# Kernel tuning notes

Hardware: AMD Instinct MI355X
Metric: run time of the kernel (lower is better)

Reference implementation:

```python
import jax, jax.numpy as jnp
import numpy as np

ALPHA_MIN = 1e-6
TAU_EPS = 1e-3


def _spectral_normalize(W):
    # spectral_norm divides by the largest singular value of W
    sigma = jnp.linalg.svd(W, compute_uv=False)[0]
    return W / sigma


def setup_inputs() -> dict:
    key = jax.random.key(0)
    ks = jax.random.split(key, 10)
    B, T, D, k = 8, 8192, 128, 64
    x = jax.random.normal(ks[0], (B, T, D), dtype=jnp.float32)
    dt = jax.random.uniform(ks[1], (B, T), dtype=jnp.float32) * (2.0 / T)
    alpha_mod = 0.1 * jax.random.normal(ks[2], (B, T, k), dtype=jnp.float32)
    omega_mod = 0.1 * jax.random.normal(ks[3], (B, T, k), dtype=jnp.float32)
    tau_mod = 0.1 * jax.random.normal(ks[4], (B, T, 1), dtype=jnp.float32)
    s_real_raw = jax.random.normal(ks[5], (k,), dtype=jnp.float32)
    s_imag = jax.random.uniform(ks[6], (k,), dtype=jnp.float32, minval=-np.pi, maxval=np.pi)
    tau_raw = jnp.zeros((), dtype=jnp.float32)
    W = jax.random.normal(ks[7], (k, D), dtype=jnp.float32) * (1.0 / np.sqrt(D))
    b = jax.random.uniform(ks[8], (k,), dtype=jnp.float32, minval=-1.0 / np.sqrt(D), maxval=1.0 / np.sqrt(D))
    return {"x": x, "dt": dt, "alpha_mod": alpha_mod, "omega_mod": omega_mod,
            "tau_mod": tau_mod, "s_real_raw": s_real_raw, "s_imag": s_imag,
            "tau_raw": tau_raw, "W": W, "b": b}


def reference(x, dt, alpha_mod, omega_mod, tau_mod, s_real_raw, s_imag, tau_raw, W, b):
    # recurrent mode of LearnableLaplacianBasis
    B, T, D = x.shape
    k = s_imag.shape[0]
    W_sn = _spectral_normalize(W)
    u = jnp.einsum('btd,kd->btk', x, W_sn) + b  # [B,T,k]

    tau = jax.nn.softplus(tau_raw) + TAU_EPS
    alpha0 = (jax.nn.softplus(s_real_raw) + ALPHA_MIN) * tau  # [k]
    omega0 = s_imag * tau                                      # [k]

    alpha = alpha0 * jnp.exp(alpha_mod)   # [B,T,k]
    omega = omega0 * jnp.exp(omega_mod)
    scale = jnp.exp(tau_mod)              # [B,T,1] broadcasts to [B,T,k]
    alpha = alpha * scale
    omega = omega * scale

    dt_bt1 = dt[:, :, None]
    rho = jnp.exp(-alpha * dt_bt1)
    theta = omega * dt_bt1
    cos_t = jnp.cos(theta)
    sin_t = jnp.sin(theta)

    # time-major for scan: [T,B,k]
    xs = (jnp.swapaxes(rho, 0, 1), jnp.swapaxes(cos_t, 0, 1),
          jnp.swapaxes(sin_t, 0, 1), jnp.swapaxes(u, 0, 1))

    def step(carry, inp):
        c, s = carry
        r, ct, st, ut = inp
        c2 = r * (c * ct - s * st) + ut
        s2 = r * (c * st + s * ct)
        return (c2, s2), (c2, s2)

    init = (jnp.zeros((B, k), x.dtype), jnp.zeros((B, k), x.dtype))
    _, (C, S) = jax.lax.scan(step, init, xs)  # [T,B,k] each
    C = jnp.swapaxes(C, 0, 1)
    S = jnp.swapaxes(S, 0, 1)
    return jnp.concatenate([C, S], axis=2)  # [B,T,2k]
```

## Files before the change

### kernel.cpp

```cpp
#include <hip/hip_runtime.h>
#include <hip/hip_bf16.h>

#define B_   8
#define T_   8192
#define D_   128
#define K_   64
#define TC   16

#define GEMM_BLOCKS 1024
#define GP 136

typedef float  floatx4  __attribute__((ext_vector_type(4)));
typedef __bf16 bf16x8   __attribute__((ext_vector_type(8)));
typedef unsigned short ushortx8 __attribute__((ext_vector_type(8)));

__device__ inline unsigned short f2bf(float f) {
  unsigned u = __float_as_uint(f);
  u = u + 0x7FFFu + ((u >> 16) & 1u);
  return (unsigned short)(u >> 16);
}
__device__ inline float bf2f(unsigned short h) {
  return __uint_as_float(((unsigned)h) << 16);
}

#define MP 72

__global__ __launch_bounds__(256) void k_gemm_sigma(
    const float* __restrict__ x, const float* __restrict__ W,
    float* __restrict__ V, float* __restrict__ sig, int* __restrict__ FL) {
  __shared__ __align__(16) unsigned char smem[2 * 64 * GP * 2 + 512];

  const int tid  = threadIdx.x;
  const int lane = tid & 63;
  const int wv   = tid >> 6;
  const int l15  = lane & 15;
  const int q    = lane >> 4;

  if (blockIdx.x == GEMM_BLOCKS) {
    FL[tid] = 0;

    unsigned short* Ma = (unsigned short*)smem;
    unsigned short* Mb = Ma + 64 * MP;
    float* red = (float*)(smem + 2 * 64 * MP * 2);
    float* vsh = red + 4;
    int*   jsh = (int*)(vsh + 64);

    floatx4 acc[4] = {};
    const int arow = 16 * wv + l15;
    for (int s = 0; s < 4; ++s) {
      const int kb = 32 * s + 8 * q;
      float4 a0 = *(const float4*)(W + arow * 128 + kb);
      float4 a1 = *(const float4*)(W + arow * 128 + kb + 4);
      ushortx8 ua;
      ua[0] = f2bf(a0.x); ua[1] = f2bf(a0.y); ua[2] = f2bf(a0.z); ua[3] = f2bf(a0.w);
      ua[4] = f2bf(a1.x); ua[5] = f2bf(a1.y); ua[6] = f2bf(a1.z); ua[7] = f2bf(a1.w);
      bf16x8 av = __builtin_bit_cast(bf16x8, ua);
      for (int tn = 0; tn < 4; ++tn) {
        const int brow = 16 * tn + l15;
        float4 b0 = *(const float4*)(W + brow * 128 + kb);
        float4 b1 = *(const float4*)(W + brow * 128 + kb + 4);
        ushortx8 ub;
        ub[0] = f2bf(b0.x); ub[1] = f2bf(b0.y); ub[2] = f2bf(b0.z); ub[3] = f2bf(b0.w);
        ub[4] = f2bf(b1.x); ub[5] = f2bf(b1.y); ub[6] = f2bf(b1.z); ub[7] = f2bf(b1.w);
        bf16x8 bv = __builtin_bit_cast(bf16x8, ub);
        acc[tn] = __builtin_amdgcn_mfma_f32_16x16x32_bf16(av, bv, acc[tn], 0, 0, 0);
      }
    }
    float mx = 0.f;
    for (int tn = 0; tn < 4; ++tn)
      for (int r = 0; r < 4; ++r) mx = fmaxf(mx, fabsf(acc[tn][r]));
    for (int off = 32; off; off >>= 1) mx = fmaxf(mx, __shfl_xor(mx, off));
    if (lane == 0) red[wv] = mx;
    __syncthreads();
    {
      float gm  = fmaxf(fmaxf(red[0], red[1]), fmaxf(red[2], red[3]));
      float inv = 1.f / gm;
      for (int tn = 0; tn < 4; ++tn)
        for (int r = 0; r < 4; ++r)
          Ma[(16 * wv + 4 * q + r) * MP + 16 * tn + l15] = f2bf(acc[tn][r] * inv);
    }
    __syncthreads();

    unsigned short* src = Ma;
    unsigned short* dst = Mb;
    for (int it = 0; it < 8; ++it) {
      floatx4 f[4] = {};
      for (int s = 0; s < 2; ++s) {
        const int kb = 32 * s + 8 * q;
        uint4 ua4 = *(const uint4*)(src + (16 * wv + l15) * MP + kb);
        bf16x8 av = __builtin_bit_cast(bf16x8, ua4);
        for (int tn = 0; tn < 4; ++tn) {
          const int n = 16 * tn + l15;
          ushortx8 ub;
          #pragma unroll
          for (int j = 0; j < 8; ++j) ub[j] = src[(kb + j) * MP + n];
          bf16x8 bv = __builtin_bit_cast(bf16x8, ub);
          f[tn] = __builtin_amdgcn_mfma_f32_16x16x32_bf16(av, bv, f[tn], 0, 0, 0);
        }
      }
      float m2 = 0.f;
      for (int tn = 0; tn < 4; ++tn)
        for (int r = 0; r < 4; ++r) m2 = fmaxf(m2, fabsf(f[tn][r]));
      for (int off = 32; off; off >>= 1) m2 = fmaxf(m2, __shfl_xor(m2, off));
      if (lane == 0) red[wv] = m2;
      __syncthreads();
      {
        float gm2  = fmaxf(fmaxf(red[0], red[1]), fmaxf(red[2], red[3]));
        float inv2 = 1.f / gm2;
        for (int tn = 0; tn < 4; ++tn)
          for (int r = 0; r < 4; ++r)
            dst[(16 * wv + 4 * q + r) * MP + 16 * tn + l15] = f2bf(f[tn][r] * inv2);
      }
      __syncthreads();
      unsigned short* t2 = src; src = dst; dst = t2;
    }

    if (tid == 0) {
      int jb = 0; float best = -1.f;
      for (int j = 0; j < 64; ++j) {
        float dv = bf2f(src[j * MP + j]);
        if (dv > best) { best = dv; jb = j; }
      }
      *jsh = jb;
    }
    __syncthreads();
    if (tid < 64) vsh[tid] = bf2f(src[tid * MP + *jsh]);
    __syncthreads();

    if (wv == 0) {
      float wa = 0.f, wb = 0.f;
      for (int i = 0; i < 64; ++i) {
        float vi = vsh[i];
        wa = fmaf(W[i * 128 + lane], vi, wa);
        wb = fmaf(W[i * 128 + 64 + lane], vi, wb);
      }
      float num = wa * wa + wb * wb;
      float den = vsh[lane] * vsh[lane];
      for (int off = 32; off; off >>= 1) {
        num += __shfl_xor(num, off);
        den += __shfl_xor(den, off);
      }
      if (lane == 0) sig[0] = 1.f / sqrtf(num / den);
    }
    return;
  }

  unsigned short* Wh = (unsigned short*)smem;
  unsigned short* Wl = Wh + 64 * GP;

  #pragma unroll
  for (int j = 0; j < 8; ++j) {
    const int v = tid + 256 * j;
    float4 w4 = ((const float4*)W)[v];
    const int e = v * 4;
    const int row = e >> 7, col = e & 127;
    float a[4] = {w4.x, w4.y, w4.z, w4.w};
    unsigned short h[4], l[4];
    #pragma unroll
    for (int i = 0; i < 4; ++i) {
      h[i] = f2bf(a[i]);
      l[i] = f2bf(a[i] - bf2f(h[i]));
    }
    unsigned hp0 = (unsigned)h[0] | ((unsigned)h[1] << 16);
    unsigned hp1 = (unsigned)h[2] | ((unsigned)h[3] << 16);
    unsigned lp0 = (unsigned)l[0] | ((unsigned)l[1] << 16);
    unsigned lp1 = (unsigned)l[2] | ((unsigned)l[3] << 16);
    *(uint2*)(Wh + row * GP + col) = make_uint2(hp0, hp1);
    *(uint2*)(Wl + row * GP + col) = make_uint2(lp0, lp1);
  }
  __syncthreads();

  const int R0 = blockIdx.x * 64 + wv * 16;
  floatx4 acc[4] = {};

  #pragma unroll
  for (int s = 0; s < 4; ++s) {
    const float* xp = x + ((size_t)(R0 + l15) << 7) + 32 * s + 8 * q;
    float4 x0 = *(const float4*)xp;
    float4 x1 = *(const float4*)(xp + 4);
    float xs8[8] = {x0.x, x0.y, x0.z, x0.w, x1.x, x1.y, x1.z, x1.w};
    ushortx8 uh, ul;
    #pragma unroll
    for (int j = 0; j < 8; ++j) {
      unsigned short h = f2bf(xs8[j]);
      uh[j] = h;
      ul[j] = f2bf(xs8[j] - bf2f(h));
    }
    bf16x8 ah = __builtin_bit_cast(bf16x8, uh);
    bf16x8 al = __builtin_bit_cast(bf16x8, ul);

    #pragma unroll
    for (int t = 0; t < 4; ++t) {
      const unsigned short* bp = Wh + (16 * t + l15) * GP + 32 * s + 8 * q;
      bf16x8 bh = __builtin_bit_cast(bf16x8, *(const uint4*)bp);
      const unsigned short* bq = Wl + (16 * t + l15) * GP + 32 * s + 8 * q;
      bf16x8 bl = __builtin_bit_cast(bf16x8, *(const uint4*)bq);
      acc[t] = __builtin_amdgcn_mfma_f32_16x16x32_bf16(ah, bh, acc[t], 0, 0, 0);
      acc[t] = __builtin_amdgcn_mfma_f32_16x16x32_bf16(al, bh, acc[t], 0, 0, 0);
      acc[t] = __builtin_amdgcn_mfma_f32_16x16x32_bf16(ah, bl, acc[t], 0, 0, 0);
    }
  }

  #pragma unroll
  for (int t = 0; t < 4; ++t)
    #pragma unroll
    for (int r = 0; r < 4; ++r)
      V[(size_t)(R0 + 4 * q + r) * 64 + 16 * t + l15] = acc[t][r];
}

__global__ __launch_bounds__(1024, 4) void k_fused(
    const float* __restrict__ am, const float* __restrict__ om,
    const float* __restrict__ tm, const float* __restrict__ dtp,
    const float* __restrict__ V,  const float* __restrict__ sr,
    const float* __restrict__ si, const float* __restrict__ traw,
    const float* __restrict__ bb, const float* __restrict__ sig,
    float* __restrict__ BA, int* __restrict__ FL,
    float* __restrict__ out) {
  __shared__ float4 sAgg[16 * 64];
  __shared__ float2 sH[64];

  const int tid  = threadIdx.x;
  const int lane = tid & 63;
  const int w    = __builtin_amdgcn_readfirstlane(tid >> 6);
  const int g    = blockIdx.x;
  const int b    = g >> 5;
  const int tb   = g & 31;
  const int gb   = g & ~31;

  const int bt0 = b * T_ + tb * 256 + w * TC;
  const float* pa = am  + (size_t)bt0 * 64 + lane;
  const float* po = om  + (size_t)bt0 * 64 + lane;
  const float* pv = V   + (size_t)bt0 * 64 + lane;

  float ca[TC], co[TC], cv[TC], ctm[TC], cdt[TC];
  #pragma unroll
  for (int t = 0; t < TC; ++t) {
    ca[t] = pa[64 * t];
    co[t] = po[64 * t];
    cv[t] = pv[64 * t];
  }
  #pragma unroll
  for (int t = 0; t < TC; ++t) {
    ctm[t] = tm[bt0 + t];
    cdt[t] = dtp[bt0 + t];
  }
  __builtin_amdgcn_sched_barrier(0);

  const float tau    = log1pf(__expf(traw[0])) + 1e-3f;
  const float alpha0 = (log1pf(__expf(sr[lane])) + 1e-6f) * tau;
  const float omega0 = si[lane] * tau;
  const float bk     = bb[lane];
  const float invs   = sig[0];

  float Ar = 1.f, Ai = 0.f, Ur = 0.f, Ui = 0.f;
  #pragma unroll
  for (int t = 0; t < TC; ++t) {
    float tmv = ctm[t];
    float dtv = cdt[t];
    float alpha = alpha0 * __expf(ca[t] + tmv);
    float omega = omega0 * __expf(co[t] + tmv);
    float rho = __expf(-alpha * dtv);
    float th  = omega * dtv;
    float th2 = th * th;
    float st  = th * fmaf(th2, -0.16666667f, 1.f);
    float ct  = fmaf(th2, -0.5f, 1.f);
    float ar  = rho * ct, ai = rho * st;
    float u   = fmaf(cv[t], invs, bk);
    ca[t] = ar; co[t] = ai; cv[t] = u;
    float nUr = fmaf(ar, Ur, fmaf(-ai, Ui, u));
    float nUi = fmaf(ar, Ui, ai * Ur);
    Ur = nUr; Ui = nUi;
    float nAr = fmaf(ar, Ar, -ai * Ai);
    float nAi = fmaf(ar, Ai, ai * Ar);
    Ar = nAr; Ai = nAi;
  }
  sAgg[w * 64 + lane] = make_float4(Ar, Ai, Ur, Ui);
  __syncthreads();

  float Er = 1.f, Ei = 0.f, Fr = 0.f, Fi = 0.f;
  #pragma unroll
  for (int j = 0; j < 15; ++j) {
    float4 a = sAgg[j * 64 + lane];
    bool p = (j < w);
    float ax = p ? a.x : 1.f;
    float ay = p ? a.y : 0.f;
    float az = p ? a.z : 0.f;
    float aw_ = p ? a.w : 0.f;
    float nEr = ax * Er - ay * Ei;
    float nEi = ax * Ei + ay * Er;
    float nFr = fmaf(ax, Fr, fmaf(-ay, Fi, az));
    float nFi = fmaf(ax, Fi, fmaf(ay, Fr, aw_));
    Er = nEr; Ei = nEi; Fr = nFr; Fi = nFi;
  }

  if (w == 15) {
    float bAr = Ar * Er - Ai * Ei;
    float bAi = Ar * Ei + Ai * Er;
    float bUr = fmaf(Ar, Fr, fmaf(-Ai, Fi, Ur));
    float bUi = fmaf(Ar, Fi, fmaf(Ai, Fr, Ui));
    *(float4*)(BA + (size_t)(g * 64 + lane) * 4) = make_float4(bAr, bAi, bUr, bUi);
  }
  __syncthreads();
  if (tid == 0) {
    __threadfence();
    __hip_atomic_store(&FL[g], 1, __ATOMIC_RELEASE, __HIP_MEMORY_SCOPE_AGENT);
  }

  if (w == 0) {
    if (lane < tb) {
      while (__hip_atomic_load(&FL[gb + lane], __ATOMIC_RELAXED,
                               __HIP_MEMORY_SCOPE_AGENT) == 0)
        __builtin_amdgcn_s_sleep(2);
    }
    __threadfence();
    float Hr = 0.f, Hi = 0.f;
    for (int j0 = 0; j0 < tb; j0 += 8) {
      float4 a[8];
      #pragma unroll
      for (int j = 0; j < 8; ++j) {
        if (j0 + j < tb)
          a[j] = *(const float4*)(BA + (size_t)((gb + j0 + j) * 64 + lane) * 4);
        else
          a[j] = make_float4(1.f, 0.f, 0.f, 0.f);
      }
      #pragma unroll
      for (int j = 0; j < 8; ++j) {
        float nHr = fmaf(a[j].x, Hr, fmaf(-a[j].y, Hi, a[j].z));
        float nHi = fmaf(a[j].x, Hi, fmaf(a[j].y, Hr, a[j].w));
        Hr = nHr; Hi = nHi;
      }
    }
    sH[lane] = make_float2(Hr, Hi);
  }
  __syncthreads();

  float2 h = sH[lane];
  float zr = fmaf(Er, h.x, fmaf(-Ei, h.y, Fr));
  float zi = fmaf(Er, h.y, fmaf(Ei, h.x, Fi));

  float* outp = out + (size_t)bt0 * 128 + lane;
  #pragma unroll
  for (int t = 0; t < TC; ++t) {
    float nr = fmaf(ca[t], zr, fmaf(-co[t], zi, cv[t]));
    float ni = fmaf(ca[t], zi, co[t] * zr);
    zr = nr; zi = ni;
    outp[0]  = zr;
    outp[64] = zi;
    outp += 128;
  }
}

extern "C" void kernel_launch(void* const* d_in, const int* in_sizes, int n_in,
                              void* d_out, int out_size, void* d_ws, size_t ws_size,
                              hipStream_t stream) {
  (void)in_sizes; (void)n_in; (void)out_size; (void)ws_size;
  const float* x    = (const float*)d_in[0];
  const float* dtp  = (const float*)d_in[1];
  const float* amod = (const float*)d_in[2];
  const float* omod = (const float*)d_in[3];
  const float* tmod = (const float*)d_in[4];
  const float* srr  = (const float*)d_in[5];
  const float* sim  = (const float*)d_in[6];
  const float* traw = (const float*)d_in[7];
  const float* W    = (const float*)d_in[8];
  const float* bb   = (const float*)d_in[9];
  float* out = (float*)d_out;
  float* ws  = (float*)d_ws;

  float* sig = ws;
  float* V   = ws + 16;
  float* BA  = V + (size_t)B_ * T_ * K_;
  int*   FL  = (int*)(BA + 256 * 64 * 4);

  k_gemm_sigma<<<GEMM_BLOCKS + 1, 256, 0, stream>>>(x, W, V, sig, FL);
  k_fused<<<256, 1024, 0, stream>>>(amod, omod, tmod, dtp, V, srr, sim, traw,
                                    bb, sig, BA, FL, out);
}
```

Measured before the change: 159.1 us.

## Fuse projection GEMM and sigma estimation into the scan kernel

Merges the GEMM and power-iteration sigma kernel into the scan kernel. Each block computes its own x·W tile with MFMA into shared memory, which removes the global round trip of the intermediate V buffer. Block 0 also computes sigma and publishes it through a release flag that the other blocks spin on. A tiny zeroing kernel resets the flags. The cost is that block 0's serial power iteration now sits on the critical path of every block waiting for sigma, and shared memory use grows to about 117 KB per block.

```diff
diff --git a/kernel.cpp b/kernel.cpp
--- a/kernel.cpp
+++ b/kernel.cpp
@@ -6,9 +6,8 @@
 #define D_   128
 #define K_   64
 #define TC   16
-
-#define GEMM_BLOCKS 1024
-#define GP 136
+#define GP   136
+#define MP   72
 
 typedef float  floatx4  __attribute__((ext_vector_type(4)));
 typedef __bf16 bf16x8   __attribute__((ext_vector_type(8)));
@@ -23,93 +22,114 @@
   return __uint_as_float(((unsigned)h) << 16);
 }
 
-#define MP 72
-
-__global__ __launch_bounds__(256) void k_gemm_sigma(
-    const float* __restrict__ x, const float* __restrict__ W,
-    float* __restrict__ V, float* __restrict__ sig, int* __restrict__ FL) {
-  __shared__ __align__(16) unsigned char smem[2 * 64 * GP * 2 + 512];
+__global__ __launch_bounds__(512) void k_zero(int* __restrict__ FL) {
+  if (threadIdx.x < 257) FL[threadIdx.x] = 0;
+}
+
+__global__ __launch_bounds__(1024, 4) void k_mega(
+    const float* __restrict__ x,  const float* __restrict__ W,
+    const float* __restrict__ am, const float* __restrict__ om,
+    const float* __restrict__ tm, const float* __restrict__ dtp,
+    const float* __restrict__ sr, const float* __restrict__ si,
+    const float* __restrict__ traw, const float* __restrict__ bb,
+    float* __restrict__ sig, float* __restrict__ BA, int* __restrict__ FL,
+    float* __restrict__ out) {
+  __shared__ __align__(16) unsigned char smem[117264];
+  unsigned short* Wh   = (unsigned short*)smem;
+  unsigned short* Wl   = Wh + 64 * GP;
+  float*          Vt   = (float*)(smem + 34816);
+  float4*         sAgg = (float4*)(smem + 100352);
+  float2*         sH   = (float2*)(smem + 116736);
+  float*          sInv = (float*)(smem + 117248);
+  unsigned short* Ma  = (unsigned short*)(smem + 34816);
+  unsigned short* Mb  = Ma + 64 * MP;
+  float*          red = (float*)(smem + 53248);
+  float*          vsh = red + 4;
+  int*            jsh = (int*)(vsh + 64);
 
   const int tid  = threadIdx.x;
   const int lane = tid & 63;
-  const int wv   = tid >> 6;
+  const int w    = __builtin_amdgcn_readfirstlane(tid >> 6);
   const int l15  = lane & 15;
   const int q    = lane >> 4;
-
-  if (blockIdx.x == GEMM_BLOCKS) {
-    FL[tid] = 0;
-
-    unsigned short* Ma = (unsigned short*)smem;
-    unsigned short* Mb = Ma + 64 * MP;
-    float* red = (float*)(smem + 2 * 64 * MP * 2);
-    float* vsh = red + 4;
-    int*   jsh = (int*)(vsh + 64);
-
-    floatx4 acc[4] = {};
-    const int arow = 16 * wv + l15;
-    for (int s = 0; s < 4; ++s) {
-      const int kb = 32 * s + 8 * q;
-      float4 a0 = *(const float4*)(W + arow * 128 + kb);
-      float4 a1 = *(const float4*)(W + arow * 128 + kb + 4);
-      ushortx8 ua;
-      ua[0] = f2bf(a0.x); ua[1] = f2bf(a0.y); ua[2] = f2bf(a0.z); ua[3] = f2bf(a0.w);
-      ua[4] = f2bf(a1.x); ua[5] = f2bf(a1.y); ua[6] = f2bf(a1.z); ua[7] = f2bf(a1.w);
-      bf16x8 av = __builtin_bit_cast(bf16x8, ua);
-      for (int tn = 0; tn < 4; ++tn) {
-        const int brow = 16 * tn + l15;
-        float4 b0 = *(const float4*)(W + brow * 128 + kb);
-        float4 b1 = *(const float4*)(W + brow * 128 + kb + 4);
-        ushortx8 ub;
-        ub[0] = f2bf(b0.x); ub[1] = f2bf(b0.y); ub[2] = f2bf(b0.z); ub[3] = f2bf(b0.w);
-        ub[4] = f2bf(b1.x); ub[5] = f2bf(b1.y); ub[6] = f2bf(b1.z); ub[7] = f2bf(b1.w);
-        bf16x8 bv = __builtin_bit_cast(bf16x8, ub);
-        acc[tn] = __builtin_amdgcn_mfma_f32_16x16x32_bf16(av, bv, acc[tn], 0, 0, 0);
-      }
-    }
-    float mx = 0.f;
-    for (int tn = 0; tn < 4; ++tn)
-      for (int r = 0; r < 4; ++r) mx = fmaxf(mx, fabsf(acc[tn][r]));
-    for (int off = 32; off; off >>= 1) mx = fmaxf(mx, __shfl_xor(mx, off));
-    if (lane == 0) red[wv] = mx;
-    __syncthreads();
+  const int g    = blockIdx.x;
+  const int b    = g >> 5;
+  const int tb   = g & 31;
+  const int gb   = g & ~31;
+
+  if (g == 0) {
+    const int wv = tid >> 6;
     {
-      float gm  = fmaxf(fmaxf(red[0], red[1]), fmaxf(red[2], red[3]));
-      float inv = 1.f / gm;
-      for (int tn = 0; tn < 4; ++tn)
-        for (int r = 0; r < 4; ++r)
-          Ma[(16 * wv + 4 * q + r) * MP + 16 * tn + l15] = f2bf(acc[tn][r] * inv);
-    }
-    __syncthreads();
+      floatx4 acc[4] = {};
+      if (tid < 256) {
+        const int arow = 16 * wv + l15;
+        for (int s = 0; s < 4; ++s) {
+          const int kb = 32 * s + 8 * q;
+          float4 a0 = *(const float4*)(W + arow * 128 + kb);
+          float4 a1 = *(const float4*)(W + arow * 128 + kb + 4);
+          ushortx8 ua;
+          ua[0] = f2bf(a0.x); ua[1] = f2bf(a0.y); ua[2] = f2bf(a0.z); ua[3] = f2bf(a0.w);
+          ua[4] = f2bf(a1.x); ua[5] = f2bf(a1.y); ua[6] = f2bf(a1.z); ua[7] = f2bf(a1.w);
+          bf16x8 av = __builtin_bit_cast(bf16x8, ua);
+          for (int tn = 0; tn < 4; ++tn) {
+            const int brow = 16 * tn + l15;
+            float4 b0 = *(const float4*)(W + brow * 128 + kb);
+            float4 b1 = *(const float4*)(W + brow * 128 + kb + 4);
+            ushortx8 ub;
+            ub[0] = f2bf(b0.x); ub[1] = f2bf(b0.y); ub[2] = f2bf(b0.z); ub[3] = f2bf(b0.w);
+            ub[4] = f2bf(b1.x); ub[5] = f2bf(b1.y); ub[6] = f2bf(b1.z); ub[7] = f2bf(b1.w);
+            bf16x8 bv = __builtin_bit_cast(bf16x8, ub);
+            acc[tn] = __builtin_amdgcn_mfma_f32_16x16x32_bf16(av, bv, acc[tn], 0, 0, 0);
+          }
+        }
+        float mx = 0.f;
+        for (int tn = 0; tn < 4; ++tn)
+          for (int r = 0; r < 4; ++r) mx = fmaxf(mx, fabsf(acc[tn][r]));
+        for (int off = 32; off; off >>= 1) mx = fmaxf(mx, __shfl_xor(mx, off));
+        if (lane == 0) red[wv] = mx;
+      }
+      __syncthreads();
+      if (tid < 256) {
+        float gm  = fmaxf(fmaxf(red[0], red[1]), fmaxf(red[2], red[3]));
+        float inv = 1.f / gm;
+        for (int tn = 0; tn < 4; ++tn)
+          for (int r = 0; r < 4; ++r)
+            Ma[(16 * wv + 4 * q + r) * MP + 16 * tn + l15] = f2bf(acc[tn][r] * inv);
+      }
+      __syncthreads();
+    }
 
     unsigned short* src = Ma;
     unsigned short* dst = Mb;
     for (int it = 0; it < 8; ++it) {
-      floatx4 f[4] = {};
-      for (int s = 0; s < 2; ++s) {
-        const int kb = 32 * s + 8 * q;
-        uint4 ua4 = *(const uint4*)(src + (16 * wv + l15) * MP + kb);
-        bf16x8 av = __builtin_bit_cast(bf16x8, ua4);
-        for (int tn = 0; tn < 4; ++tn) {
-          const int n = 16 * tn + l15;
-          ushortx8 ub;
-          #pragma unroll
-          for (int j = 0; j < 8; ++j) ub[j] = src[(kb + j) * MP + n];
-          bf16x8 bv = __builtin_bit_cast(bf16x8, ub);
-          f[tn] = __builtin_amdgcn_mfma_f32_16x16x32_bf16(av, bv, f[tn], 0, 0, 0);
+      if (tid < 256) {
+        floatx4 f[4] = {};
+        for (int s = 0; s < 2; ++s) {
+          const int kb = 32 * s + 8 * q;
+          uint4 ua4 = *(const uint4*)(src + (16 * wv + l15) * MP + kb);
+          bf16x8 av = __builtin_bit_cast(bf16x8, ua4);
+          for (int tn = 0; tn < 4; ++tn) {
+            const int n = 16 * tn + l15;
+            ushortx8 ub;
+            #pragma unroll
+            for (int j = 0; j < 8; ++j) ub[j] = src[(kb + j) * MP + n];
+            bf16x8 bv = __builtin_bit_cast(bf16x8, ub);
+            f[tn] = __builtin_amdgcn_mfma_f32_16x16x32_bf16(av, bv, f[tn], 0, 0, 0);
+          }
         }
-      }
-      float m2 = 0.f;
-      for (int tn = 0; tn < 4; ++tn)
-        for (int r = 0; r < 4; ++r) m2 = fmaxf(m2, fabsf(f[tn][r]));
-      for (int off = 32; off; off >>= 1) m2 = fmaxf(m2, __shfl_xor(m2, off));
-      if (lane == 0) red[wv] = m2;
-      __syncthreads();
-      {
+        float m2 = 0.f;
+        for (int tn = 0; tn < 4; ++tn)
+          for (int r = 0; r < 4; ++r) m2 = fmaxf(m2, fabsf(f[tn][r]));
+        for (int off = 32; off; off >>= 1) m2 = fmaxf(m2, __shfl_xor(m2, off));
+        if (lane == 0) red[wv] = m2;
+        __syncthreads();
         float gm2  = fmaxf(fmaxf(red[0], red[1]), fmaxf(red[2], red[3]));
         float inv2 = 1.f / gm2;
         for (int tn = 0; tn < 4; ++tn)
           for (int r = 0; r < 4; ++r)
             dst[(16 * wv + 4 * q + r) * MP + 16 * tn + l15] = f2bf(f[tn][r] * inv2);
+      } else {
+        __syncthreads();
       }
       __syncthreads();
       unsigned short* t2 = src; src = dst; dst = t2;
@@ -126,15 +146,14 @@
     __syncthreads();
     if (tid < 64) vsh[tid] = bf2f(src[tid * MP + *jsh]);
     __syncthreads();
-
-    if (wv == 0) {
-      float wa = 0.f, wb = 0.f;
+    if (tid < 64) {
+      float wa = 0.f, wb2 = 0.f;
       for (int i = 0; i < 64; ++i) {
         float vi = vsh[i];
-        wa = fmaf(W[i * 128 + lane], vi, wa);
-        wb = fmaf(W[i * 128 + 64 + lane], vi, wb);
-      }
-      float num = wa * wa + wb * wb;
+        wa  = fmaf(W[i * 128 + lane], vi, wa);
+        wb2 = fmaf(W[i * 128 + 64 + lane], vi, wb2);
+      }
+      float num = wa * wa + wb2 * wb2;
       float den = vsh[lane] * vsh[lane];
       for (int off = 32; off; off >>= 1) {
         num += __shfl_xor(num, off);
@@ -142,15 +161,16 @@
       }
       if (lane == 0) sig[0] = 1.f / sqrtf(num / den);
     }
-    return;
-  }
-
-  unsigned short* Wh = (unsigned short*)smem;
-  unsigned short* Wl = Wh + 64 * GP;
-
-  #pragma unroll
-  for (int j = 0; j < 8; ++j) {
-    const int v = tid + 256 * j;
+    if (tid == 0) {
+      __threadfence();
+      __hip_atomic_store(&FL[256], 1, __ATOMIC_RELEASE, __HIP_MEMORY_SCOPE_AGENT);
+    }
+    __syncthreads();
+  }
+
+  #pragma unroll
+  for (int j = 0; j < 2; ++j) {
+    const int v = tid + 1024 * j;
     float4 w4 = ((const float4*)W)[v];
     const int e = v * 4;
     const int row = e >> 7, col = e & 127;
@@ -170,87 +190,72 @@
   }
   __syncthreads();
 
-  const int R0 = blockIdx.x * 64 + wv * 16;
-  floatx4 acc[4] = {};
-
-  #pragma unroll
-  for (int s = 0; s < 4; ++s) {
-    const float* xp = x + ((size_t)(R0 + l15) << 7) + 32 * s + 8 * q;
-    float4 x0 = *(const float4*)xp;
-    float4 x1 = *(const float4*)(xp + 4);
-    float xs8[8] = {x0.x, x0.y, x0.z, x0.w, x1.x, x1.y, x1.z, x1.w};
-    ushortx8 uh, ul;
+  const int bt0 = b * T_ + tb * 256 + w * TC;
+  float* Vw = Vt + w * 1024;
+  {
+    floatx4 acc[4] = {};
     #pragma unroll
-    for (int j = 0; j < 8; ++j) {
-      unsigned short h = f2bf(xs8[j]);
-      uh[j] = h;
-      ul[j] = f2bf(xs8[j] - bf2f(h));
-    }
-    bf16x8 ah = __builtin_bit_cast(bf16x8, uh);
-    bf16x8 al = __builtin_bit_cast(bf16x8, ul);
-
+    for (int s = 0; s < 4; ++s) {
+      const float* xp = x + ((size_t)(bt0 + l15) << 7) + 32 * s + 8 * q;
+      float4 x0 = *(const float4*)xp;
+      float4 x1 = *(const float4*)(xp + 4);
+      float xs8[8] = {x0.x, x0.y, x0.z, x0.w, x1.x, x1.y, x1.z, x1.w};
+      ushortx8 uh, ul;
+      #pragma unroll
+      for (int j = 0; j < 8; ++j) {
+        unsigned short h = f2bf(xs8[j]);
+        uh[j] = h;
+        ul[j] = f2bf(xs8[j] - bf2f(h));
+      }
+      bf16x8 ah = __builtin_bit_cast(bf16x8, uh);
+      bf16x8 al = __builtin_bit_cast(bf16x8, ul);
+      #pragma unroll
+      for (int t = 0; t < 4; ++t) {
+        const unsigned short* bp = Wh + (16 * t + l15) * GP + 32 * s + 8 * q;
+        bf16x8 bh = __builtin_bit_cast(bf16x8, *(const uint4*)bp);
+        const unsigned short* bq = Wl + (16 * t + l15) * GP + 32 * s + 8 * q;
+        bf16x8 bl = __builtin_bit_cast(bf16x8, *(const uint4*)bq);
+        acc[t] = __builtin_amdgcn_mfma_f32_16x16x32_bf16(ah, bh, acc[t], 0, 0, 0);
+        acc[t] = __builtin_amdgcn_mfma_f32_16x16x32_bf16(al, bh, acc[t], 0, 0, 0);
+        acc[t] = __builtin_amdgcn_mfma_f32_16x16x32_bf16(ah, bl, acc[t], 0, 0, 0);
+      }
+    }
     #pragma unroll
-    for (int t = 0; t < 4; ++t) {
-      const unsigned short* bp = Wh + (16 * t + l15) * GP + 32 * s + 8 * q;
-      bf16x8 bh = __builtin_bit_cast(bf16x8, *(const uint4*)bp);
-      const unsigned short* bq = Wl + (16 * t + l15) * GP + 32 * s + 8 * q;
-      bf16x8 bl = __builtin_bit_cast(bf16x8, *(const uint4*)bq);
-      acc[t] = __builtin_amdgcn_mfma_f32_16x16x32_bf16(ah, bh, acc[t], 0, 0, 0);
-      acc[t] = __builtin_amdgcn_mfma_f32_16x16x32_bf16(al, bh, acc[t], 0, 0, 0);
-      acc[t] = __builtin_amdgcn_mfma_f32_16x16x32_bf16(ah, bl, acc[t], 0, 0, 0);
-    }
-  }
-
-  #pragma unroll
-  for (int t = 0; t < 4; ++t)
-    #pragma unroll
-    for (int r = 0; r < 4; ++r)
-      V[(size_t)(R0 + 4 * q + r) * 64 + 16 * t + l15] = acc[t][r];
-}
-
-__global__ __launch_bounds__(1024, 4) void k_fused(
-    const float* __restrict__ am, const float* __restrict__ om,
-    const float* __restrict__ tm, const float* __restrict__ dtp,
-    const float* __restrict__ V,  const float* __restrict__ sr,
-    const float* __restrict__ si, const float* __restrict__ traw,
-    const float* __restrict__ bb, const float* __restrict__ sig,
-    float* __restrict__ BA, int* __restrict__ FL,
-    float* __restrict__ out) {
-  __shared__ float4 sAgg[16 * 64];
-  __shared__ float2 sH[64];
-
-  const int tid  = threadIdx.x;
-  const int lane = tid & 63;
-  const int w    = __builtin_amdgcn_readfirstlane(tid >> 6);
-  const int g    = blockIdx.x;
-  const int b    = g >> 5;
-  const int tb   = g & 31;
-  const int gb   = g & ~31;
-
-  const int bt0 = b * T_ + tb * 256 + w * TC;
-  const float* pa = am  + (size_t)bt0 * 64 + lane;
-  const float* po = om  + (size_t)bt0 * 64 + lane;
-  const float* pv = V   + (size_t)bt0 * 64 + lane;
-
-  float ca[TC], co[TC], cv[TC], ctm[TC], cdt[TC];
-  #pragma unroll
-  for (int t = 0; t < TC; ++t) {
-    ca[t] = pa[64 * t];
-    co[t] = po[64 * t];
-    cv[t] = pv[64 * t];
-  }
-  #pragma unroll
-  for (int t = 0; t < TC; ++t) {
-    ctm[t] = tm[bt0 + t];
-    cdt[t] = dtp[bt0 + t];
-  }
-  __builtin_amdgcn_sched_barrier(0);
+    for (int t = 0; t < 4; ++t)
+      #pragma unroll
+      for (int r = 0; r < 4; ++r)
+        Vw[(4 * q + r) * 64 + 16 * t + l15] = acc[t][r];
+  }
+
+  if (tid == 0) {
+    while (__hip_atomic_load(&FL[256], __ATOMIC_RELAXED,
+                             __HIP_MEMORY_SCOPE_AGENT) == 0)
+      __builtin_amdgcn_s_sleep(2);
+    __threadfence();
+    sInv[0] = sig[0];
+  }
+  __syncthreads();
+  const float invs = sInv[0];
 
   const float tau    = log1pf(__expf(traw[0])) + 1e-3f;
   const float alpha0 = (log1pf(__expf(sr[lane])) + 1e-6f) * tau;
   const float omega0 = si[lane] * tau;
   const float bk     = bb[lane];
-  const float invs   = sig[0];
+
+  const float* pa = am + (size_t)bt0 * 64 + lane;
+  const float* po = om + (size_t)bt0 * 64 + lane;
+  float ca[TC], co[TC], ctm[TC], cdt[TC];
+  #pragma unroll
+  for (int t = 0; t < TC; ++t) {
+    ca[t] = pa[64 * t];
+    co[t] = po[64 * t];
+  }
+  #pragma unroll
+  for (int t = 0; t < TC; ++t) {
+    ctm[t] = tm[bt0 + t];
+    cdt[t] = dtp[bt0 + t];
+  }
+  __builtin_amdgcn_sched_barrier(0);
 
   float Ar = 1.f, Ai = 0.f, Ur = 0.f, Ui = 0.f;
   #pragma unroll
@@ -265,8 +270,9 @@
     float st  = th * fmaf(th2, -0.16666667f, 1.f);
     float ct  = fmaf(th2, -0.5f, 1.f);
     float ar  = rho * ct, ai = rho * st;
-    float u   = fmaf(cv[t], invs, bk);
-    ca[t] = ar; co[t] = ai; cv[t] = u;
+    float u   = fmaf(Vw[t * 64 + lane], invs, bk);
+    Vw[t * 64 + lane] = u;
+    ca[t] = ar; co[t] = ai;
     float nUr = fmaf(ar, Ur, fmaf(-ai, Ui, u));
     float nUi = fmaf(ar, Ui, ai * Ur);
     Ur = nUr; Ui = nUi;
@@ -341,7 +347,8 @@
   float* outp = out + (size_t)bt0 * 128 + lane;
   #pragma unroll
   for (int t = 0; t < TC; ++t) {
-    float nr = fmaf(ca[t], zr, fmaf(-co[t], zi, cv[t]));
+    float u  = Vw[t * 64 + lane];
+    float nr = fmaf(ca[t], zr, fmaf(-co[t], zi, u));
     float ni = fmaf(ca[t], zi, co[t] * zr);
     zr = nr; zi = ni;
     outp[0]  = zr;
@@ -368,11 +375,10 @@
   float* ws  = (float*)d_ws;
 
   float* sig = ws;
-  float* V   = ws + 16;
-  float* BA  = V + (size_t)B_ * T_ * K_;
+  float* BA  = ws + 16;
   int*   FL  = (int*)(BA + 256 * 64 * 4);
 
-  k_gemm_sigma<<<GEMM_BLOCKS + 1, 256, 0, stream>>>(x, W, V, sig, FL);
-  k_fused<<<256, 1024, 0, stream>>>(amod, omod, tmod, dtp, V, srr, sim, traw,
-                                    bb, sig, BA, FL, out);
-}
+  k_zero<<<1, 512, 0, stream>>>(FL);
+  k_mega<<<256, 1024, 0, stream>>>(x, W, amod, omod, tmod, dtp, srr, sim,
+                                   traw, bb, sig, BA, FL, out);
+}
```

New measurement: 160.3 us. Within noise of the previous version (+0.7%).
